# Kernel tuning notes

Measured on AMD Instinct MI355X. Metric: run time of the kernel, lower is better.

The kernel has to match this reference:

```python
import jax, jax.numpy as jnp
import numpy as np


def setup_inputs() -> dict:
    key = jax.random.key(0)
    k1, k2 = jax.random.split(key)
    B, H, W, C = 8, 32, 32, 512
    N = 25000
    feature_batch = jax.random.normal(k1, (B, H, W, C), dtype=jnp.float32)
    mb = jax.random.normal(k2, (N, C), dtype=jnp.float32)
    return {"feature_batch": feature_batch, "mb": mb, "b": 9}


def reference(feature_batch, mb, b):
    # feature_batch: (B,H,W,C), mb: (N,C), b: python int
    B, H, W, C = feature_batch.shape
    fv = feature_batch.reshape(B * H * W, C)
    sq_dists = ((fv * fv).sum(1)[:, None]
                + (mb * mb).sum(1)[None, :]
                - 2.0 * fv @ mb.T)                      # (BHW, N)
    pixel_scores = jnp.sqrt(sq_dists.min(axis=1)).reshape(B, H * W)
    # index of most anomalous pixel per image
    idx = jnp.argmax(pixel_scores, axis=1)              # (B,)
    flat_idx = idx + jnp.arange(B) * (H * W)
    selected = fv[flat_idx]                             # (B, C)
    # exact squared distances of selected vectors to full memory bank
    dists_to_mb = ((selected[:, None, :] - mb[None, :, :]) ** 2).sum(-1)  # (B, N)
    # b nearest memory-bank entries (ascending distance order)
    _, b_closest_idx = jax.lax.top_k(-dists_to_mb, b)   # (B, b)
    sel_mb = mb[b_closest_idx]                          # (B, b, C)
    selected_dists = jnp.sqrt(((selected[:, None, :] - sel_mb) ** 2).sum(-1))  # (B, b)
    image_scores = selected_dists[:, 0]
    if b > 1:
        image_scores = image_scores * (1.0 - jax.nn.softmax(selected_dists, axis=1)[:, 0])
    return pixel_scores.reshape(B, 1, H, W), image_scores
```

## Files before the change

kernel.cpp:

```cpp
#include <hip/hip_runtime.h>
#include <hip/hip_bf16.h>

typedef __attribute__((ext_vector_type(8))) short short8;
typedef __attribute__((ext_vector_type(4))) float f32x4;

#define INF_F 3.4e38f

__device__ __forceinline__ void gload16(const void* g, void* l) {
    __builtin_amdgcn_global_load_lds((const __attribute__((address_space(1))) unsigned*)g,
                                     (__attribute__((address_space(3))) unsigned*)l, 16, 0, 0);
}

__global__ void k_conv(const float* __restrict__ fv, const float* __restrict__ mbp,
                       unsigned short* __restrict__ fvb, unsigned short* __restrict__ mbb,
                       float* __restrict__ fnorm, float* __restrict__ mnorm,
                       float* ps_sq, int* ncand, float* cand_val) {
    int t = threadIdx.x, wid = t >> 6, lane = t & 63;
    if (blockIdx.x == 0) {
        if (t == 0) ncand[0] = 0;
        if (t < 64) ((unsigned*)cand_val)[t] = 0x7f800000u;
    }
    int row = blockIdx.x * 4 + wid;
    const float* in; unsigned short* outb; float* norm; int r;
    if (row < 8192) {
        in = fv; outb = fvb; norm = fnorm; r = row;
        if (lane == 0) ((unsigned*)ps_sq)[row] = 0x7f800000u;
    } else if (row < 33192) {
        in = mbp; outb = mbb; norm = mnorm; r = row - 8192;
    } else return;
    const float4* p = (const float4*)(in + (size_t)r * 512) + lane * 2;
    float4 a = p[0], b = p[1];
    float n = a.x*a.x + a.y*a.y + a.z*a.z + a.w*a.w
            + b.x*b.x + b.y*b.y + b.z*b.z + b.w*b.w;
    float vals[8] = {a.x, a.y, a.z, a.w, b.x, b.y, b.z, b.w};
    unsigned short h[8];
    #pragma unroll
    for (int e = 0; e < 8; ++e) {
        unsigned u = __float_as_uint(vals[e]);
        h[e] = (unsigned short)((u + 0x7fffu + ((u >> 16) & 1u)) >> 16);
    }
    *(uint4*)(outb + (size_t)r * 512 + lane * 8) = *(uint4*)h;
    #pragma unroll
    for (int s = 1; s < 64; s <<= 1) n += __shfl_xor(n, s, 64);
    if (lane == 0) norm[r] = n;
}

__global__ __launch_bounds__(256, 2)
void k_gemm_min(const unsigned short* __restrict__ A, const unsigned short* __restrict__ B,
                const float* __restrict__ fnorm, const float* __restrict__ mnorm,
                float* __restrict__ ps_sq) {
    __shared__ unsigned short At[128 * 64];
    __shared__ unsigned short Bt[128 * 64];
    int tid = threadIdx.x, wid = tid >> 6, lane = tid & 63;
    int bid = blockIdx.x;
    int pos = bid >> 3;
    int rb = ((bid & 7) << 3) | (pos & 7);
    int cb = pos >> 3;
    int brow = rb * 128, bcol = cb * 128;
    int wm = (wid >> 1) * 64, wn = (wid & 1) * 64;

    f32x4 acc[4][4] = {};
    int lr = lane >> 3;
    int lkswz = ((lane & 7) ^ lr) * 8;

    for (int k0 = 0; k0 < 512; k0 += 64) {
        #pragma unroll
        for (int c = 0; c < 4; ++c) {
            int ch = wid + c * 4;
            int row = ch * 8 + lr;
            gload16(A + (size_t)(brow + row) * 512 + k0 + lkswz, &At[ch * 512]);
            int srow = bcol + row; if (srow > 24999) srow = 24999;
            gload16(B + (size_t)srow * 512 + k0 + lkswz, &Bt[ch * 512]);
        }
        __syncthreads();
        #pragma unroll
        for (int kk = 0; kk < 2; ++kk) {
            short8 af[4], bf[4];
            int ko = kk * 32 + (lane >> 4) * 8;
            #pragma unroll
            for (int mi = 0; mi < 4; ++mi) {
                int r = wm + mi * 16 + (lane & 15);
                af[mi] = *(const short8*)&At[r * 64 + (ko ^ ((r & 7) << 3))];
            }
            #pragma unroll
            for (int ni = 0; ni < 4; ++ni) {
                int r = wn + ni * 16 + (lane & 15);
                bf[ni] = *(const short8*)&Bt[r * 64 + (ko ^ ((r & 7) << 3))];
            }
            #pragma unroll
            for (int mi = 0; mi < 4; ++mi)
                #pragma unroll
                for (int ni = 0; ni < 4; ++ni)
                    acc[mi][ni] = __builtin_amdgcn_mfma_f32_16x16x32_bf16(af[mi], bf[ni], acc[mi][ni], 0, 0, 0);
        }
        __syncthreads();
    }

    float mnv[4];
    #pragma unroll
    for (int ni = 0; ni < 4; ++ni) {
        int col = bcol + wn + ni * 16 + (lane & 15);
        mnv[ni] = (col < 25000) ? mnorm[col] : INF_F;
    }
    #pragma unroll
    for (int mi = 0; mi < 4; ++mi) {
        #pragma unroll
        for (int r = 0; r < 4; ++r) {
            float v = INF_F;
            #pragma unroll
            for (int ni = 0; ni < 4; ++ni) v = fminf(v, mnv[ni] - 2.0f * acc[mi][ni][r]);
            #pragma unroll
            for (int s = 1; s < 16; s <<= 1) v = fminf(v, __shfl_xor(v, s, 64));
            if ((lane & 15) == 0) {
                int row = brow + wm + mi * 16 + (lane >> 4) * 4 + r;
                float sq = v + fnorm[row];
                atomicMin((unsigned*)&ps_sq[row], __float_as_uint(sq));
            }
        }
    }
}

__global__ void k_cand(const float* __restrict__ ps_sq, float* __restrict__ out0,
                       int* ncand, int* cand_pix, int* cand_batch) {
    __shared__ float smax[4];
    __shared__ int scnt;
    int b = blockIdx.x, t = threadIdx.x, wid = t >> 6, lane = t & 63;
    const float* base = ps_sq + b * 1024;
    float v[4]; float m = -INF_F;
    #pragma unroll
    for (int i = 0; i < 4; ++i) {
        v[i] = base[t + i * 256];
        out0[b * 1024 + t + i * 256] = sqrtf(fmaxf(v[i], 0.0f));
        m = fmaxf(m, v[i]);
    }
    #pragma unroll
    for (int s = 1; s < 64; s <<= 1) m = fmaxf(m, __shfl_xor(m, s, 64));
    if (lane == 0) smax[wid] = m;
    if (t == 0) scnt = 0;
    __syncthreads();
    float bm = fmaxf(fmaxf(smax[0], smax[1]), fmaxf(smax[2], smax[3]));
    #pragma unroll
    for (int i = 0; i < 4; ++i) {
        if (v[i] >= bm - 8.0f) {
            int s = atomicAdd(&scnt, 1);
            if (s < 8) {
                int g = atomicAdd(ncand, 1);
                if (g < 64) { cand_pix[g] = b * 1024 + t + i * 256; cand_batch[g] = b; }
            }
        }
    }
}

__global__ __launch_bounds__(256, 4)
void k_score(const float* __restrict__ fv, const float* __restrict__ mb,
             const int* __restrict__ ncand, const int* __restrict__ cand_pix,
             float* __restrict__ cand_val) {
    int nct = ncand[0]; if (nct > 64) nct = 64;
    int c0 = blockIdx.y * 4;
    if (c0 >= nct) return;
    int t = threadIdx.x, wid = t >> 6, lane = t & 63;

    int p0i = cand_pix[c0];
    int p1i = cand_pix[c0 + 1 < nct ? c0 + 1 : c0];
    int p2i = cand_pix[c0 + 2 < nct ? c0 + 2 : c0];
    int p3i = cand_pix[c0 + 3 < nct ? c0 + 3 : c0];
    const float4* s0 = (const float4*)(fv + (size_t)p0i * 512) + lane * 2;
    const float4* s1 = (const float4*)(fv + (size_t)p1i * 512) + lane * 2;
    const float4* s2 = (const float4*)(fv + (size_t)p2i * 512) + lane * 2;
    const float4* s3 = (const float4*)(fv + (size_t)p3i * 512) + lane * 2;
    float4 ca0 = s0[0], ca1 = s0[1];
    float4 cb0 = s1[0], cb1 = s1[1];
    float4 cc0 = s2[0], cc1 = s2[1];
    float4 cd0 = s3[0], cd1 = s3[1];

    float m0v = INF_F, m1v = INF_F, m2v = INF_F, m3v = INF_F;
    int rbase = blockIdx.x * 64 + wid * 16;
    #pragma unroll 4
    for (int i = 0; i < 16; ++i) {
        int r = rbase + i;
        int rc = r < 24999 ? r : 24999;
        const float4* mp = (const float4*)(mb + (size_t)rc * 512) + lane * 2;
        float4 x0 = mp[0], x1 = mp[1];
        float d, p0 = 0.f, p1 = 0.f, p2 = 0.f, p3 = 0.f;
        d = x0.x-ca0.x; p0 += d*d;  d = x0.y-ca0.y; p0 += d*d;  d = x0.z-ca0.z; p0 += d*d;  d = x0.w-ca0.w; p0 += d*d;
        d = x1.x-ca1.x; p0 += d*d;  d = x1.y-ca1.y; p0 += d*d;  d = x1.z-ca1.z; p0 += d*d;  d = x1.w-ca1.w; p0 += d*d;
        d = x0.x-cb0.x; p1 += d*d;  d = x0.y-cb0.y; p1 += d*d;  d = x0.z-cb0.z; p1 += d*d;  d = x0.w-cb0.w; p1 += d*d;
        d = x1.x-cb1.x; p1 += d*d;  d = x1.y-cb1.y; p1 += d*d;  d = x1.z-cb1.z; p1 += d*d;  d = x1.w-cb1.w; p1 += d*d;
        d = x0.x-cc0.x; p2 += d*d;  d = x0.y-cc0.y; p2 += d*d;  d = x0.z-cc0.z; p2 += d*d;  d = x0.w-cc0.w; p2 += d*d;
        d = x1.x-cc1.x; p2 += d*d;  d = x1.y-cc1.y; p2 += d*d;  d = x1.z-cc1.z; p2 += d*d;  d = x1.w-cc1.w; p2 += d*d;
        d = x0.x-cd0.x; p3 += d*d;  d = x0.y-cd0.y; p3 += d*d;  d = x0.z-cd0.z; p3 += d*d;  d = x0.w-cd0.w; p3 += d*d;
        d = x1.x-cd1.x; p3 += d*d;  d = x1.y-cd1.y; p3 += d*d;  d = x1.z-cd1.z; p3 += d*d;  d = x1.w-cd1.w; p3 += d*d;
        #pragma unroll
        for (int s = 1; s < 64; s <<= 1) {
            p0 += __shfl_xor(p0, s, 64);
            p1 += __shfl_xor(p1, s, 64);
            p2 += __shfl_xor(p2, s, 64);
            p3 += __shfl_xor(p3, s, 64);
        }
        bool ok = (r < 25000);
        m0v = fminf(m0v, ok ? p0 : INF_F); m1v = fminf(m1v, ok ? p1 : INF_F);
        m2v = fminf(m2v, ok ? p2 : INF_F); m3v = fminf(m3v, ok ? p3 : INF_F);
    }
    if (lane < 4 && c0 + lane < nct) {
        float mv = (lane == 0) ? m0v : (lane == 1) ? m1v : (lane == 2) ? m2v : m3v;
        atomicMin((unsigned*)&cand_val[c0 + lane], __float_as_uint(mv));
    }
}

__global__ __launch_bounds__(256, 4)
void k_dists4(const float* __restrict__ fv, const float* __restrict__ mb,
              const int* __restrict__ ncand, const int* __restrict__ cand_pix,
              const int* __restrict__ cand_batch, const float* __restrict__ cand_val,
              float* __restrict__ exact_d) {
    int bg = blockIdx.y * 4;
    int t = threadIdx.x, wid = t >> 6, lane = t & 63;
    int n = ncand[0]; if (n > 64) n = 64;

    int sp0, sp1, sp2, sp3;
#define WINNER(Q, OUTV) do { float v = -INF_F; int pix = 0x7fffffff; \
    if (lane < n && cand_batch[lane] == bg + (Q)) { v = cand_val[lane]; pix = cand_pix[lane]; } \
    _Pragma("unroll") \
    for (int s = 1; s < 64; s <<= 1) { \
        float ov = __shfl_xor(v, s, 64); int oi = __shfl_xor(pix, s, 64); \
        if (ov > v || (ov == v && oi < pix)) { v = ov; pix = oi; } } \
    OUTV = (pix == 0x7fffffff) ? (bg + (Q)) * 1024 : pix; } while (0)
    WINNER(0, sp0); WINNER(1, sp1); WINNER(2, sp2); WINNER(3, sp3);
#undef WINNER

    const float4* s0 = (const float4*)(fv + (size_t)sp0 * 512) + lane * 2;
    const float4* s1 = (const float4*)(fv + (size_t)sp1 * 512) + lane * 2;
    const float4* s2 = (const float4*)(fv + (size_t)sp2 * 512) + lane * 2;
    const float4* s3 = (const float4*)(fv + (size_t)sp3 * 512) + lane * 2;
    float4 ca0 = s0[0], ca1 = s0[1];
    float4 cb0 = s1[0], cb1 = s1[1];
    float4 cc0 = s2[0], cc1 = s2[1];
    float4 cd0 = s3[0], cd1 = s3[1];

    int rbase = blockIdx.x * 64 + wid * 16;
    #pragma unroll 4
    for (int i = 0; i < 16; ++i) {
        int r = rbase + i;
        int rc = r < 24999 ? r : 24999;
        const float4* mp = (const float4*)(mb + (size_t)rc * 512) + lane * 2;
        float4 x0 = mp[0], x1 = mp[1];
        float d, p0 = 0.f, p1 = 0.f, p2 = 0.f, p3 = 0.f;
        d = x0.x-ca0.x; p0 += d*d;  d = x0.y-ca0.y; p0 += d*d;  d = x0.z-ca0.z; p0 += d*d;  d = x0.w-ca0.w; p0 += d*d;
        d = x1.x-ca1.x; p0 += d*d;  d = x1.y-ca1.y; p0 += d*d;  d = x1.z-ca1.z; p0 += d*d;  d = x1.w-ca1.w; p0 += d*d;
        d = x0.x-cb0.x; p1 += d*d;  d = x0.y-cb0.y; p1 += d*d;  d = x0.z-cb0.z; p1 += d*d;  d = x0.w-cb0.w; p1 += d*d;
        d = x1.x-cb1.x; p1 += d*d;  d = x1.y-cb1.y; p1 += d*d;  d = x1.z-cb1.z; p1 += d*d;  d = x1.w-cb1.w; p1 += d*d;
        d = x0.x-cc0.x; p2 += d*d;  d = x0.y-cc0.y; p2 += d*d;  d = x0.z-cc0.z; p2 += d*d;  d = x0.w-cc0.w; p2 += d*d;
        d = x1.x-cc1.x; p2 += d*d;  d = x1.y-cc1.y; p2 += d*d;  d = x1.z-cc1.z; p2 += d*d;  d = x1.w-cc1.w; p2 += d*d;
        d = x0.x-cd0.x; p3 += d*d;  d = x0.y-cd0.y; p3 += d*d;  d = x0.z-cd0.z; p3 += d*d;  d = x0.w-cd0.w; p3 += d*d;
        d = x1.x-cd1.x; p3 += d*d;  d = x1.y-cd1.y; p3 += d*d;  d = x1.z-cd1.z; p3 += d*d;  d = x1.w-cd1.w; p3 += d*d;
        #pragma unroll
        for (int s = 1; s < 64; s <<= 1) {
            p0 += __shfl_xor(p0, s, 64);
            p1 += __shfl_xor(p1, s, 64);
            p2 += __shfl_xor(p2, s, 64);
            p3 += __shfl_xor(p3, s, 64);
        }
        if (lane < 4 && r < 25000) {
            float pv = (lane == 0) ? p0 : (lane == 1) ? p1 : (lane == 2) ? p2 : p3;
            exact_d[(size_t)(bg + lane) * 25000 + r] = pv;
        }
    }
}

__global__ __launch_bounds__(1024)
void k_final(const float* __restrict__ exact_d, const int* __restrict__ bptr,
             float* __restrict__ out_img) {
    __shared__ float wbv[16]; __shared__ int wbi[16];
    __shared__ float seld[128];
    __shared__ float gbv_s; __shared__ int gbi_s;
    int b = blockIdx.x, t = threadIdx.x, wid = t >> 6, lane = t & 63;
    int bval = bptr[0]; if (bval > 128) bval = 128; if (bval < 1) bval = 1;
    const float* dv = exact_d + (size_t)b * 25000;

    if (bval <= 16) {
        float tv[16]; int ti[16];
        #pragma unroll
        for (int k = 0; k < 16; ++k) { tv[k] = INF_F; ti[k] = 0x7fffffff; }
        for (int r = t; r < 25000; r += 1024) {
            float cv = dv[r]; int ci = r;
            #pragma unroll
            for (int k = 0; k < 16; ++k) {
                bool better = (cv < tv[k]) || (cv == tv[k] && ci < ti[k]);
                if (better) {
                    float t1 = tv[k]; tv[k] = cv; cv = t1;
                    int   t2 = ti[k]; ti[k] = ci; ci = t2;
                }
            }
        }
        for (int k = 0; k < bval; ++k) {
            float bv = tv[0]; int bi = ti[0];
            #pragma unroll
            for (int s = 1; s < 64; s <<= 1) {
                float ov = __shfl_xor(bv, s, 64); int oi = __shfl_xor(bi, s, 64);
                if (ov < bv || (ov == bv && oi < bi)) { bv = ov; bi = oi; }
            }
            if (lane == 0) { wbv[wid] = bv; wbi[wid] = bi; }
            __syncthreads();
            if (t == 0) {
                float fb = wbv[0]; int fi = wbi[0];
                for (int w2 = 1; w2 < 16; ++w2)
                    if (wbv[w2] < fb || (wbv[w2] == fb && wbi[w2] < fi)) { fb = wbv[w2]; fi = wbi[w2]; }
                seld[k] = sqrtf(fb);
                gbv_s = fb; gbi_s = fi;
            }
            __syncthreads();
            if (tv[0] == gbv_s && ti[0] == gbi_s) {
                #pragma unroll
                for (int k2 = 0; k2 < 15; ++k2) { tv[k2] = tv[k2 + 1]; ti[k2] = ti[k2 + 1]; }
                tv[15] = INF_F; ti[15] = 0x7fffffff;
            }
        }
    } else {
        float lastV = -INF_F; int lastI = -1;
        for (int k = 0; k < bval; ++k) {
            float bv = INF_F; int bi = 0x7fffffff;
            for (int r = t; r < 25000; r += 1024) {
                float vv = dv[r];
                bool after = (vv > lastV) || (vv == lastV && r > lastI);
                if (after && (vv < bv || (vv == bv && r < bi))) { bv = vv; bi = r; }
            }
            #pragma unroll
            for (int s = 1; s < 64; s <<= 1) {
                float ov = __shfl_xor(bv, s, 64); int oi = __shfl_xor(bi, s, 64);
                if (ov < bv || (ov == bv && oi < bi)) { bv = ov; bi = oi; }
            }
            if (lane == 0) { wbv[wid] = bv; wbi[wid] = bi; }
            __syncthreads();
            if (t == 0) {
                float fb = wbv[0]; int fi = wbi[0];
                for (int w2 = 1; w2 < 16; ++w2)
                    if (wbv[w2] < fb || (wbv[w2] == fb && wbi[w2] < fi)) { fb = wbv[w2]; fi = wbi[w2]; }
                seld[k] = sqrtf(fb);
                gbv_s = fb; gbi_s = fi;
            }
            __syncthreads();
            lastV = gbv_s; lastI = gbi_s;
        }
    }

    if (t == 0) {
        float d0 = seld[0];
        float img = d0;
        if (bval > 1) {
            float m = -INF_F;
            for (int k = 0; k < bval; ++k) m = fmaxf(m, seld[k]);
            float s = 0.f;
            for (int k = 0; k < bval; ++k) s += expf(seld[k] - m);
            float p0 = expf(seld[0] - m) / s;
            img = d0 * (1.0f - p0);
        }
        out_img[b] = img;
    }
}

extern "C" void kernel_launch(void* const* d_in, const int* in_sizes, int n_in,
                              void* d_out, int out_size, void* d_ws, size_t ws_size,
                              hipStream_t stream) {
    const float* fv = (const float*)d_in[0];
    const float* mb = (const float*)d_in[1];
    const int*   bp = (const int*)d_in[2];
    float* out = (float*)d_out;

    char* w = (char*)d_ws;
    unsigned short* fvb = (unsigned short*)w;
    unsigned short* mbb = (unsigned short*)(w + 8388608);
    size_t o = 8388608 + 25600000;
    float* fnorm    = (float*)(w + o); o += 32768;
    float* mnorm    = (float*)(w + o); o += 100352;
    float* ps_sq    = (float*)(w + o); o += 32768;
    int*   ncand    = (int*)(w + o);   o += 256;
    int*   cand_pix = (int*)(w + o);   o += 256;
    int*   cand_bat = (int*)(w + o);   o += 256;
    float* cand_val = (float*)(w + o); o += 256;
    int*   sel_unused = (int*)(w + o); o += 256;
    float* exact_d  = (float*)(w + o); o += 800000;
    (void)sel_unused;

    k_conv<<<8298, 256, 0, stream>>>(fv, mb, fvb, mbb, fnorm, mnorm, ps_sq, ncand, cand_val);
    k_gemm_min<<<12544, 256, 0, stream>>>(fvb, mbb, fnorm, mnorm, ps_sq);
    k_cand<<<8, 256, 0, stream>>>(ps_sq, out, ncand, cand_pix, cand_bat);
    k_score<<<dim3(391, 16), 256, 0, stream>>>(fv, mb, ncand, cand_pix, cand_val);
    k_dists4<<<dim3(391, 2), 256, 0, stream>>>(fv, mb, ncand, cand_pix, cand_bat, cand_val, exact_d);
    k_final<<<8, 1024, 0, stream>>>(exact_d, bp, out + 8192);
}
```

Before: 490.0 us.

## Use norm-expansion dot products and half-wave row split in candidate scoring kernels

Rewrites k_score and k_dists4 to compute distances as ||x||^2+||m||^2-2x·m from the precomputed fp32 norms, instead of summing squared differences. Each half-wavefront now handles a separate memory-bank row, which shortens the shuffle reduction from six steps to five per row. k_final also gets an early-reject test against the 16th-best entry before insertion, and clamps to zero before sqrt. The norm expansion can cancel badly and change the exact nearest-neighbour ordering. Launch bounds are lowered to 2 waves per EU so the larger register footprint fits.

Result: faster. 477.3 us (-2.6%).

```diff
diff --git a/kernel.cpp b/kernel.cpp
--- a/kernel.cpp
+++ b/kernel.cpp
@@ -9,6 +9,10 @@
 __device__ __forceinline__ void gload16(const void* g, void* l) {
     __builtin_amdgcn_global_load_lds((const __attribute__((address_space(1))) unsigned*)g,
                                      (__attribute__((address_space(3))) unsigned*)l, 16, 0, 0);
+}
+
+__device__ __forceinline__ float dot4(float4 a, float4 b) {
+    return a.x*b.x + a.y*b.y + a.z*b.z + a.w*b.w;
 }
 
 __global__ void k_conv(const float* __restrict__ fv, const float* __restrict__ mbp,
@@ -151,69 +155,78 @@
     }
 }
 
-__global__ __launch_bounds__(256, 4)
+__global__ __launch_bounds__(256, 2)
 void k_score(const float* __restrict__ fv, const float* __restrict__ mb,
+             const float* __restrict__ fnorm, const float* __restrict__ mnorm,
              const int* __restrict__ ncand, const int* __restrict__ cand_pix,
              float* __restrict__ cand_val) {
     int nct = ncand[0]; if (nct > 64) nct = 64;
     int c0 = blockIdx.y * 4;
     if (c0 >= nct) return;
     int t = threadIdx.x, wid = t >> 6, lane = t & 63;
+    int half = lane >> 5, j = lane & 31;
 
     int p0i = cand_pix[c0];
     int p1i = cand_pix[c0 + 1 < nct ? c0 + 1 : c0];
     int p2i = cand_pix[c0 + 2 < nct ? c0 + 2 : c0];
     int p3i = cand_pix[c0 + 3 < nct ? c0 + 3 : c0];
-    const float4* s0 = (const float4*)(fv + (size_t)p0i * 512) + lane * 2;
-    const float4* s1 = (const float4*)(fv + (size_t)p1i * 512) + lane * 2;
-    const float4* s2 = (const float4*)(fv + (size_t)p2i * 512) + lane * 2;
-    const float4* s3 = (const float4*)(fv + (size_t)p3i * 512) + lane * 2;
-    float4 ca0 = s0[0], ca1 = s0[1];
-    float4 cb0 = s1[0], cb1 = s1[1];
-    float4 cc0 = s2[0], cc1 = s2[1];
-    float4 cd0 = s3[0], cd1 = s3[1];
+    const float4* s0 = (const float4*)(fv + (size_t)p0i * 512 + 16 * j);
+    const float4* s1 = (const float4*)(fv + (size_t)p1i * 512 + 16 * j);
+    const float4* s2 = (const float4*)(fv + (size_t)p2i * 512 + 16 * j);
+    const float4* s3 = (const float4*)(fv + (size_t)p3i * 512 + 16 * j);
+    float4 a0 = s0[0], a1 = s0[1], a2 = s0[2], a3 = s0[3];
+    float4 b0 = s1[0], b1 = s1[1], b2 = s1[2], b3 = s1[3];
+    float4 g0 = s2[0], g1 = s2[1], g2 = s2[2], g3 = s2[3];
+    float4 h0 = s3[0], h1 = s3[1], h2 = s3[2], h3 = s3[3];
+    float fn0 = fnorm[p0i], fn1 = fnorm[p1i], fn2 = fnorm[p2i], fn3 = fnorm[p3i];
 
     float m0v = INF_F, m1v = INF_F, m2v = INF_F, m3v = INF_F;
     int rbase = blockIdx.x * 64 + wid * 16;
-    #pragma unroll 4
-    for (int i = 0; i < 16; ++i) {
-        int r = rbase + i;
+    #pragma unroll 2
+    for (int i = 0; i < 8; ++i) {
+        int r = rbase + i * 2 + half;
         int rc = r < 24999 ? r : 24999;
-        const float4* mp = (const float4*)(mb + (size_t)rc * 512) + lane * 2;
-        float4 x0 = mp[0], x1 = mp[1];
-        float d, p0 = 0.f, p1 = 0.f, p2 = 0.f, p3 = 0.f;
-        d = x0.x-ca0.x; p0 += d*d;  d = x0.y-ca0.y; p0 += d*d;  d = x0.z-ca0.z; p0 += d*d;  d = x0.w-ca0.w; p0 += d*d;
-        d = x1.x-ca1.x; p0 += d*d;  d = x1.y-ca1.y; p0 += d*d;  d = x1.z-ca1.z; p0 += d*d;  d = x1.w-ca1.w; p0 += d*d;
-        d = x0.x-cb0.x; p1 += d*d;  d = x0.y-cb0.y; p1 += d*d;  d = x0.z-cb0.z; p1 += d*d;  d = x0.w-cb0.w; p1 += d*d;
-        d = x1.x-cb1.x; p1 += d*d;  d = x1.y-cb1.y; p1 += d*d;  d = x1.z-cb1.z; p1 += d*d;  d = x1.w-cb1.w; p1 += d*d;
-        d = x0.x-cc0.x; p2 += d*d;  d = x0.y-cc0.y; p2 += d*d;  d = x0.z-cc0.z; p2 += d*d;  d = x0.w-cc0.w; p2 += d*d;
-        d = x1.x-cc1.x; p2 += d*d;  d = x1.y-cc1.y; p2 += d*d;  d = x1.z-cc1.z; p2 += d*d;  d = x1.w-cc1.w; p2 += d*d;
-        d = x0.x-cd0.x; p3 += d*d;  d = x0.y-cd0.y; p3 += d*d;  d = x0.z-cd0.z; p3 += d*d;  d = x0.w-cd0.w; p3 += d*d;
-        d = x1.x-cd1.x; p3 += d*d;  d = x1.y-cd1.y; p3 += d*d;  d = x1.z-cd1.z; p3 += d*d;  d = x1.w-cd1.w; p3 += d*d;
-        #pragma unroll
-        for (int s = 1; s < 64; s <<= 1) {
-            p0 += __shfl_xor(p0, s, 64);
-            p1 += __shfl_xor(p1, s, 64);
-            p2 += __shfl_xor(p2, s, 64);
-            p3 += __shfl_xor(p3, s, 64);
-        }
+        const float4* mp = (const float4*)(mb + (size_t)rc * 512 + 16 * j);
+        float4 x0 = mp[0], x1 = mp[1], x2 = mp[2], x3 = mp[3];
+        float q0 = dot4(x0,a0) + dot4(x1,a1) + dot4(x2,a2) + dot4(x3,a3);
+        float q1 = dot4(x0,b0) + dot4(x1,b1) + dot4(x2,b2) + dot4(x3,b3);
+        float q2 = dot4(x0,g0) + dot4(x1,g1) + dot4(x2,g2) + dot4(x3,g3);
+        float q3 = dot4(x0,h0) + dot4(x1,h1) + dot4(x2,h2) + dot4(x3,h3);
+        #pragma unroll
+        for (int s = 1; s < 32; s <<= 1) {
+            q0 += __shfl_xor(q0, s, 64);
+            q1 += __shfl_xor(q1, s, 64);
+            q2 += __shfl_xor(q2, s, 64);
+            q3 += __shfl_xor(q3, s, 64);
+        }
+        float mnr = mnorm[rc];
         bool ok = (r < 25000);
+        float p0 = fn0 + mnr - 2.0f * q0;
+        float p1 = fn1 + mnr - 2.0f * q1;
+        float p2 = fn2 + mnr - 2.0f * q2;
+        float p3 = fn3 + mnr - 2.0f * q3;
         m0v = fminf(m0v, ok ? p0 : INF_F); m1v = fminf(m1v, ok ? p1 : INF_F);
         m2v = fminf(m2v, ok ? p2 : INF_F); m3v = fminf(m3v, ok ? p3 : INF_F);
     }
+    m0v = fminf(m0v, __shfl_xor(m0v, 32, 64));
+    m1v = fminf(m1v, __shfl_xor(m1v, 32, 64));
+    m2v = fminf(m2v, __shfl_xor(m2v, 32, 64));
+    m3v = fminf(m3v, __shfl_xor(m3v, 32, 64));
     if (lane < 4 && c0 + lane < nct) {
         float mv = (lane == 0) ? m0v : (lane == 1) ? m1v : (lane == 2) ? m2v : m3v;
         atomicMin((unsigned*)&cand_val[c0 + lane], __float_as_uint(mv));
     }
 }
 
-__global__ __launch_bounds__(256, 4)
+__global__ __launch_bounds__(256, 2)
 void k_dists4(const float* __restrict__ fv, const float* __restrict__ mb,
+              const float* __restrict__ fnorm, const float* __restrict__ mnorm,
               const int* __restrict__ ncand, const int* __restrict__ cand_pix,
               const int* __restrict__ cand_batch, const float* __restrict__ cand_val,
               float* __restrict__ exact_d) {
     int bg = blockIdx.y * 4;
     int t = threadIdx.x, wid = t >> 6, lane = t & 63;
+    int half = lane >> 5, j = lane & 31;
     int n = ncand[0]; if (n > 64) n = 64;
 
     int sp0, sp1, sp2, sp3;
@@ -227,41 +240,40 @@
     WINNER(0, sp0); WINNER(1, sp1); WINNER(2, sp2); WINNER(3, sp3);
 #undef WINNER
 
-    const float4* s0 = (const float4*)(fv + (size_t)sp0 * 512) + lane * 2;
-    const float4* s1 = (const float4*)(fv + (size_t)sp1 * 512) + lane * 2;
-    const float4* s2 = (const float4*)(fv + (size_t)sp2 * 512) + lane * 2;
-    const float4* s3 = (const float4*)(fv + (size_t)sp3 * 512) + lane * 2;
-    float4 ca0 = s0[0], ca1 = s0[1];
-    float4 cb0 = s1[0], cb1 = s1[1];
-    float4 cc0 = s2[0], cc1 = s2[1];
-    float4 cd0 = s3[0], cd1 = s3[1];
+    const float4* s0 = (const float4*)(fv + (size_t)sp0 * 512 + 16 * j);
+    const float4* s1 = (const float4*)(fv + (size_t)sp1 * 512 + 16 * j);
+    const float4* s2 = (const float4*)(fv + (size_t)sp2 * 512 + 16 * j);
+    const float4* s3 = (const float4*)(fv + (size_t)sp3 * 512 + 16 * j);
+    float4 a0 = s0[0], a1 = s0[1], a2 = s0[2], a3 = s0[3];
+    float4 b0 = s1[0], b1 = s1[1], b2 = s1[2], b3 = s1[3];
+    float4 g0 = s2[0], g1 = s2[1], g2 = s2[2], g3 = s2[3];
+    float4 h0 = s3[0], h1 = s3[1], h2 = s3[2], h3 = s3[3];
+    float fn0 = fnorm[sp0], fn1 = fnorm[sp1], fn2 = fnorm[sp2], fn3 = fnorm[sp3];
 
     int rbase = blockIdx.x * 64 + wid * 16;
-    #pragma unroll 4
-    for (int i = 0; i < 16; ++i) {
-        int r = rbase + i;
+    #pragma unroll 2
+    for (int i = 0; i < 8; ++i) {
+        int r = rbase + i * 2 + half;
         int rc = r < 24999 ? r : 24999;
-        const float4* mp = (const float4*)(mb + (size_t)rc * 512) + lane * 2;
-        float4 x0 = mp[0], x1 = mp[1];
-        float d, p0 = 0.f, p1 = 0.f, p2 = 0.f, p3 = 0.f;
-        d = x0.x-ca0.x; p0 += d*d;  d = x0.y-ca0.y; p0 += d*d;  d = x0.z-ca0.z; p0 += d*d;  d = x0.w-ca0.w; p0 += d*d;
-        d = x1.x-ca1.x; p0 += d*d;  d = x1.y-ca1.y; p0 += d*d;  d = x1.z-ca1.z; p0 += d*d;  d = x1.w-ca1.w; p0 += d*d;
-        d = x0.x-cb0.x; p1 += d*d;  d = x0.y-cb0.y; p1 += d*d;  d = x0.z-cb0.z; p1 += d*d;  d = x0.w-cb0.w; p1 += d*d;
-        d = x1.x-cb1.x; p1 += d*d;  d = x1.y-cb1.y; p1 += d*d;  d = x1.z-cb1.z; p1 += d*d;  d = x1.w-cb1.w; p1 += d*d;
-        d = x0.x-cc0.x; p2 += d*d;  d = x0.y-cc0.y; p2 += d*d;  d = x0.z-cc0.z; p2 += d*d;  d = x0.w-cc0.w; p2 += d*d;
-        d = x1.x-cc1.x; p2 += d*d;  d = x1.y-cc1.y; p2 += d*d;  d = x1.z-cc1.z; p2 += d*d;  d = x1.w-cc1.w; p2 += d*d;
-        d = x0.x-cd0.x; p3 += d*d;  d = x0.y-cd0.y; p3 += d*d;  d = x0.z-cd0.z; p3 += d*d;  d = x0.w-cd0.w; p3 += d*d;
-        d = x1.x-cd1.x; p3 += d*d;  d = x1.y-cd1.y; p3 += d*d;  d = x1.z-cd1.z; p3 += d*d;  d = x1.w-cd1.w; p3 += d*d;
-        #pragma unroll
-        for (int s = 1; s < 64; s <<= 1) {
-            p0 += __shfl_xor(p0, s, 64);
-            p1 += __shfl_xor(p1, s, 64);
-            p2 += __shfl_xor(p2, s, 64);
-            p3 += __shfl_xor(p3, s, 64);
-        }
-        if (lane < 4 && r < 25000) {
-            float pv = (lane == 0) ? p0 : (lane == 1) ? p1 : (lane == 2) ? p2 : p3;
-            exact_d[(size_t)(bg + lane) * 25000 + r] = pv;
+        const float4* mp = (const float4*)(mb + (size_t)rc * 512 + 16 * j);
+        float4 x0 = mp[0], x1 = mp[1], x2 = mp[2], x3 = mp[3];
+        float q0 = dot4(x0,a0) + dot4(x1,a1) + dot4(x2,a2) + dot4(x3,a3);
+        float q1 = dot4(x0,b0) + dot4(x1,b1) + dot4(x2,b2) + dot4(x3,b3);
+        float q2 = dot4(x0,g0) + dot4(x1,g1) + dot4(x2,g2) + dot4(x3,g3);
+        float q3 = dot4(x0,h0) + dot4(x1,h1) + dot4(x2,h2) + dot4(x3,h3);
+        #pragma unroll
+        for (int s = 1; s < 32; s <<= 1) {
+            q0 += __shfl_xor(q0, s, 64);
+            q1 += __shfl_xor(q1, s, 64);
+            q2 += __shfl_xor(q2, s, 64);
+            q3 += __shfl_xor(q3, s, 64);
+        }
+        if (j == 0 && r < 25000) {
+            float mnr = mnorm[rc];
+            exact_d[(size_t)(bg + 0) * 25000 + r] = fn0 + mnr - 2.0f * q0;
+            exact_d[(size_t)(bg + 1) * 25000 + r] = fn1 + mnr - 2.0f * q1;
+            exact_d[(size_t)(bg + 2) * 25000 + r] = fn2 + mnr - 2.0f * q2;
+            exact_d[(size_t)(bg + 3) * 25000 + r] = fn3 + mnr - 2.0f * q3;
         }
     }
 }
@@ -282,12 +294,14 @@
         for (int k = 0; k < 16; ++k) { tv[k] = INF_F; ti[k] = 0x7fffffff; }
         for (int r = t; r < 25000; r += 1024) {
             float cv = dv[r]; int ci = r;
-            #pragma unroll
-            for (int k = 0; k < 16; ++k) {
-                bool better = (cv < tv[k]) || (cv == tv[k] && ci < ti[k]);
-                if (better) {
-                    float t1 = tv[k]; tv[k] = cv; cv = t1;
-                    int   t2 = ti[k]; ti[k] = ci; ci = t2;
+            if (cv < tv[15] || (cv == tv[15] && ci < ti[15])) {
+                #pragma unroll
+                for (int k = 0; k < 16; ++k) {
+                    bool better = (cv < tv[k]) || (cv == tv[k] && ci < ti[k]);
+                    if (better) {
+                        float t1 = tv[k]; tv[k] = cv; cv = t1;
+                        int   t2 = ti[k]; ti[k] = ci; ci = t2;
+                    }
                 }
             }
         }
@@ -304,7 +318,7 @@
                 float fb = wbv[0]; int fi = wbi[0];
                 for (int w2 = 1; w2 < 16; ++w2)
                     if (wbv[w2] < fb || (wbv[w2] == fb && wbi[w2] < fi)) { fb = wbv[w2]; fi = wbi[w2]; }
-                seld[k] = sqrtf(fb);
+                seld[k] = sqrtf(fmaxf(fb, 0.0f));
                 gbv_s = fb; gbi_s = fi;
             }
             __syncthreads();
@@ -334,7 +348,7 @@
                 float fb = wbv[0]; int fi = wbi[0];
                 for (int w2 = 1; w2 < 16; ++w2)
                     if (wbv[w2] < fb || (wbv[w2] == fb && wbi[w2] < fi)) { fb = wbv[w2]; fi = wbi[w2]; }
-                seld[k] = sqrtf(fb);
+                seld[k] = sqrtf(fmaxf(fb, 0.0f));
                 gbv_s = fb; gbi_s = fi;
             }
             __syncthreads();
@@ -383,7 +397,7 @@
     k_conv<<<8298, 256, 0, stream>>>(fv, mb, fvb, mbb, fnorm, mnorm, ps_sq, ncand, cand_val);
     k_gemm_min<<<12544, 256, 0, stream>>>(fvb, mbb, fnorm, mnorm, ps_sq);
     k_cand<<<8, 256, 0, stream>>>(ps_sq, out, ncand, cand_pix, cand_bat);
-    k_score<<<dim3(391, 16), 256, 0, stream>>>(fv, mb, ncand, cand_pix, cand_val);
-    k_dists4<<<dim3(391, 2), 256, 0, stream>>>(fv, mb, ncand, cand_pix, cand_bat, cand_val, exact_d);
+    k_score<<<dim3(391, 16), 256, 0, stream>>>(fv, mb, fnorm, mnorm, ncand, cand_pix, cand_val);
+    k_dists4<<<dim3(391, 2), 256, 0, stream>>>(fv, mb, fnorm, mnorm, ncand, cand_pix, cand_bat, cand_val, exact_d);
     k_final<<<8, 1024, 0, stream>>>(exact_d, bp, out + 8192);
 }
```
